# Optimization experiments

Measured on AMD Instinct MI355X. Metric: run time of the kernel, lower is better.

Reference implementation:

```python
import jax, jax.numpy as jnp
import numpy as np

N, E, B, DIM = 10000, 100000, 64, 64
NF, EF, H = 92, 50, 128
N_CONV, STEPS = 2, 2


def setup_inputs() -> dict:
    key = jax.random.key(0)
    ks = jax.random.split(key, 16)
    r = lambda k, s: jax.random.normal(k, s, dtype=jnp.float32) * 0.05
    return {
        "x": jax.random.normal(ks[0], (N, NF), dtype=jnp.float32),
        "edge_attr": jax.random.normal(ks[1], (E, EF), dtype=jnp.float32),
        "lin0_w": r(ks[2], (DIM, NF)), "lin0_b": jnp.zeros((DIM,), jnp.float32),
        "nn1_w": r(ks[3], (H, EF)), "nn1_b": jnp.zeros((H,), jnp.float32),
        "nn2_w": r(ks[4], (DIM * DIM, H)), "nn2_b": jnp.zeros((DIM * DIM,), jnp.float32),
        "root": r(ks[5], (DIM, DIM)), "conv_bias": jnp.zeros((DIM,), jnp.float32),
        "gru_w_ih": r(ks[6], (3 * DIM, DIM)), "gru_w_hh": r(ks[7], (3 * DIM, DIM)),
        "gru_b_ih": jnp.zeros((3 * DIM,), jnp.float32), "gru_b_hh": jnp.zeros((3 * DIM,), jnp.float32),
        "lstm_w_ih": r(ks[8], (4 * DIM, 2 * DIM)), "lstm_w_hh": r(ks[9], (4 * DIM, DIM)),
        "lstm_b_ih": jnp.zeros((4 * DIM,), jnp.float32), "lstm_b_hh": jnp.zeros((4 * DIM,), jnp.float32),
        "lin1_w": r(ks[10], (DIM, 2 * DIM)), "lin1_b": jnp.zeros((DIM,), jnp.float32),
        "lin2_w": r(ks[11], (1, DIM)), "lin2_b": jnp.zeros((1,), jnp.float32),
        "edge_index": jax.random.randint(ks[12], (2, E), 0, N),
        "batch": jnp.sort(jax.random.randint(ks[13], (N,), 0, B)),
    }


def _forward(x, edge_attr, lin0_w, lin0_b, nn1_w, nn1_b, nn2_w, nn2_b, root, conv_bias,
             gru_w_ih, gru_w_hh, gru_b_ih, gru_b_hh, lstm_w_ih, lstm_w_hh, lstm_b_ih, lstm_b_hh,
             lin1_w, lin1_b, lin2_w, lin2_b, edge_index, batch):
    src, dst = edge_index[0], edge_index[1]
    out = jax.nn.relu(x @ lin0_w.T + lin0_b)            # [N, DIM]
    h = out                                              # GRU hidden state (h0 = out)
    # Edge-conditioned weights depend only on edge_attr; identical each conv step.
    he = jax.nn.relu(edge_attr @ nn1_w.T + nn1_b)        # [E, H]
    We = (he @ nn2_w.T + nn2_b).reshape(E, DIM, DIM)     # [E, DIM, DIM]
    deg = jax.ops.segment_sum(jnp.ones((E,), jnp.float32), dst, num_segments=N)
    inv_deg = jnp.where(deg > 0, 1.0 / jnp.maximum(deg, 1.0), 0.0)[:, None]
    for _ in range(N_CONV):
        msg = jnp.einsum('ei,eio->eo', out[src], We)     # per-edge matvec, [E, DIM]
        agg = jax.ops.segment_sum(msg, dst, num_segments=N) * inv_deg  # scatter-mean
        m = jax.nn.relu(agg + out @ root + conv_bias)
        # GRU cell (torch gate order: r, z, n)
        gx = m @ gru_w_ih.T + gru_b_ih
        gh = h @ gru_w_hh.T + gru_b_hh
        xr, xz, xn = jnp.split(gx, 3, axis=-1)
        hr, hz, hn = jnp.split(gh, 3, axis=-1)
        rg = jax.nn.sigmoid(xr + hr)
        zg = jax.nn.sigmoid(xz + hz)
        ng = jnp.tanh(xn + rg * hn)
        h = (1.0 - zg) * ng + zg * h
        out = h
    # Set2Set pooling
    q_star = jnp.zeros((B, 2 * DIM), jnp.float32)
    hs = jnp.zeros((B, DIM), jnp.float32)
    cs = jnp.zeros((B, DIM), jnp.float32)
    for _ in range(STEPS):
        gates = q_star @ lstm_w_ih.T + lstm_b_ih + hs @ lstm_w_hh.T + lstm_b_hh
        ig, fg, gg, og = jnp.split(gates, 4, axis=-1)    # torch gate order i,f,g,o
        cs = jax.nn.sigmoid(fg) * cs + jax.nn.sigmoid(ig) * jnp.tanh(gg)
        hs = jax.nn.sigmoid(og) * jnp.tanh(cs)
        q = hs                                           # [B, DIM]
        e = jnp.sum(out * q[batch], axis=-1)             # [N]
        emax = jax.ops.segment_max(e, batch, num_segments=B)
        ee = jnp.exp(e - emax[batch])
        denom = jax.ops.segment_sum(ee, batch, num_segments=B)
        a = ee / jnp.maximum(denom, 1e-16)[batch]        # per-graph softmax
        rvec = jax.ops.segment_sum(a[:, None] * out, batch, num_segments=B)
        q_star = jnp.concatenate([q, rvec], axis=-1)     # [B, 2*DIM]
    y = jax.nn.relu(q_star @ lin1_w.T + lin1_b) @ lin2_w.T + lin2_b
    return y.reshape(-1)                                 # [B]


def reference(x, edge_attr, lin0_w, lin0_b, nn1_w, nn1_b, nn2_w, nn2_b, root, conv_bias,
              gru_w_ih, gru_w_hh, gru_b_ih, gru_b_hh, lstm_w_ih, lstm_w_hh, lstm_b_ih, lstm_b_hh,
              lin1_w, lin1_b, lin2_w, lin2_b, edge_index, batch):
    return _forward(x, edge_attr, lin0_w, lin0_b, nn1_w, nn1_b, nn2_w, nn2_b, root, conv_bias,
                    gru_w_ih, gru_w_hh, gru_b_ih, gru_b_hh, lstm_w_ih, lstm_w_hh, lstm_b_ih, lstm_b_hh,
                    lin1_w, lin1_b, lin2_w, lin2_b, edge_index, batch)
```

## Files before the change

kernel.cpp:

```cpp
#include <hip/hip_runtime.h>
#include <hip/hip_bf16.h>

#define N_   10000
#define E_   100000
#define B_   64
#define DIM_ 64
#define NF_  92
#define EF_  50
#define H_   128
#define NPAD 10048

typedef unsigned int u32;
typedef unsigned short u16;
typedef __attribute__((ext_vector_type(8))) short s16x8;
typedef __attribute__((ext_vector_type(4))) float f32x4;

__device__ __forceinline__ float sigm(float x) { return 1.f / (1.f + __expf(-x)); }
__device__ __forceinline__ float rdlane(float v, int l) {
  return __uint_as_float(__builtin_amdgcn_readlane(__float_as_uint(v), l));
}
__device__ __forceinline__ float bf2f(u16 u) {
  return __uint_as_float(((u32)u) << 16);
}
__device__ __forceinline__ u16 f2bf(float f) {
  u32 u = __float_as_uint(f);
  u32 r = (u + 0x7FFFu + ((u >> 16) & 1u)) >> 16;
  return (u16)r;
}

__global__ __launch_bounds__(256) void k_lin0(const float* __restrict__ x,
                                              const float* __restrict__ w,
                                              const float* __restrict__ b,
                                              float* __restrict__ out) {
  __shared__ float xs[4][NF_];
  __shared__ float w_s[DIM_][93];
  int n0 = blockIdx.x << 2;
  int tid = threadIdx.x;
  for (int k = tid; k < 4 * NF_; k += 256) {
    int nl = k / NF_, f = k % NF_;
    xs[nl][f] = x[(size_t)(n0 + nl) * NF_ + f];
  }
  for (int g = tid; g < DIM_ * NF_; g += 256) {
    int d = g / NF_, f = g % NF_;
    w_s[d][f] = w[g];
  }
  __syncthreads();
  int nl = tid >> 6, d = tid & 63;
  float acc = b[d];
  for (int f = 0; f < NF_; ++f) acc += xs[nl][f] * w_s[d][f];
  out[(size_t)(n0 + nl) * DIM_ + d] = fmaxf(acc, 0.f);
}

__global__ __launch_bounds__(256) void k_he(const float* __restrict__ ea,
                                            const float* __restrict__ w,
                                            const float* __restrict__ b,
                                            float* __restrict__ he) {
  __shared__ float wt[EF_][132];
  __shared__ float es[32][52];
  int e0 = blockIdx.x * 32, t = threadIdx.x;
  for (int g = t; g < H_ * EF_; g += 256) {
    int h = g / EF_, f = g % EF_;
    wt[f][h] = w[g];
  }
  for (int g = t; g < 32 * EF_; g += 256) {
    int e = g / EF_, f = g % EF_;
    es[e][f] = ea[(size_t)(e0 + e) * EF_ + f];
  }
  __syncthreads();
  int h0 = (t & 31) << 2, eg = t >> 5;
  float acc[4][4];
#pragma unroll
  for (int j = 0; j < 4; ++j)
#pragma unroll
    for (int c = 0; c < 4; ++c) acc[j][c] = b[h0 + c];
  for (int f = 0; f < EF_; ++f) {
    float4 wv = *(const float4*)&wt[f][h0];
    const float* wp = (const float*)&wv;
#pragma unroll
    for (int j = 0; j < 4; ++j) {
      float ev = es[eg * 4 + j][f];
#pragma unroll
      for (int c = 0; c < 4; ++c) acc[j][c] = fmaf(ev, wp[c], acc[j][c]);
    }
  }
#pragma unroll
  for (int j = 0; j < 4; ++j) {
    float4 o;
    o.x = fmaxf(acc[j][0], 0.f); o.y = fmaxf(acc[j][1], 0.f);
    o.z = fmaxf(acc[j][2], 0.f); o.w = fmaxf(acc[j][3], 0.f);
    *(float4*)&he[(size_t)(e0 + eg * 4 + j) * H_ + h0] = o;
  }
}

__global__ __launch_bounds__(256) void k_hist(const int* __restrict__ ei,
                                              int* __restrict__ outcnt,
                                              float* __restrict__ degf) {
  int e = blockIdx.x * 256 + threadIdx.x;
  if (e < E_) {
    atomicAdd(&outcnt[ei[e]], 1);
    atomicAdd(&degf[ei[E_ + e]], 1.0f);
  }
}

__global__ __launch_bounds__(1024) void k_scan(const int* __restrict__ outcnt,
                                               int* __restrict__ estart,
                                               int* __restrict__ cursor) {
  __shared__ int part[1024];
  int t = threadIdx.x;
  int base = t * 10;
  int c[10];
  int s = 0;
#pragma unroll
  for (int j = 0; j < 10; ++j) {
    int idx = base + j;
    c[j] = (idx < N_) ? outcnt[idx] : 0;
    s += c[j];
  }
  part[t] = s;
  __syncthreads();
  for (int off = 1; off < 1024; off <<= 1) {
    int v = (t >= off) ? part[t - off] : 0;
    __syncthreads();
    part[t] += v;
    __syncthreads();
  }
  int ex = (t > 0) ? part[t - 1] : 0;
#pragma unroll
  for (int j = 0; j < 10; ++j) {
    int idx = base + j;
    if (idx < N_) { estart[idx] = ex; cursor[idx] = ex; }
    ex += c[j];
  }
  if (t == 1023) estart[N_] = part[1023];
}

__global__ __launch_bounds__(256) void k_scatter(const int* __restrict__ ei,
                                                 int* __restrict__ cursor,
                                                 int* __restrict__ eorder) {
  int e = blockIdx.x * 256 + threadIdx.x;
  if (e < E_) {
    int s = ei[e];
    int pos = atomicAdd(&cursor[s], 1);
    eorder[pos] = e;
  }
}

__global__ __launch_bounds__(256) void k_gstart(const int* __restrict__ batch,
                                                int* __restrict__ gs) {
  int n = blockIdx.x * 256 + threadIdx.x;
  if (n >= N_) return;
  int b = batch[n];
  if (n == 0) {
    for (int bb = 0; bb <= b; ++bb) gs[bb] = 0;
  } else {
    int pb = batch[n - 1];
    if (pb != b)
      for (int bb = pb + 1; bb <= b; ++bb) gs[bb] = n;
  }
  if (n == N_ - 1) {
    for (int bb = b + 1; bb <= B_; ++bb) gs[bb] = N_;
  }
}

__global__ __launch_bounds__(256) void k_transpose(const float* __restrict__ gih,
                                                   const float* __restrict__ ghh,
                                                   const float* __restrict__ lih,
                                                   const float* __restrict__ lhh,
                                                   float* __restrict__ gihT,
                                                   float* __restrict__ ghhT,
                                                   float* __restrict__ lihT,
                                                   float* __restrict__ lhhT) {
  int idx = blockIdx.x * 256 + threadIdx.x;
  if (idx < 192 * 64) {
    int r = idx >> 6, i = idx & 63;
    gihT[i * 192 + r] = gih[idx];
    ghhT[i * 192 + r] = ghh[idx];
  }
  if (idx < 256 * 128) {
    int r = idx >> 7, k = idx & 127;
    lihT[k * 256 + r] = lih[idx];
  }
  if (idx < 256 * 64) {
    int r = idx >> 6, k = idx & 63;
    lhhT[k * 256 + r] = lhh[idx];
  }
}

__global__ __launch_bounds__(256) void k_prep_w(const float* __restrict__ w,
                                                u16* __restrict__ bth,
                                                u16* __restrict__ btl,
                                                int CW) {
  int idx = blockIdx.x * 256 + threadIdx.x;
  if (idx >= 64 * 64 * 128) return;
  int h = idx & 127;
  int io = idx >> 7;
  int o = io & 63;
  int i = io >> 6;
  int chunk = h / CW, hl = h % CW;
  float v = w[idx];
  u16 hh = f2bf(v);
  float r = v - bf2f(hh);
  size_t dst = (size_t)chunk * CW * 4096 + ((size_t)(hl * 64 + o)) * 64 + i;
  bth[dst] = hh;
  btl[dst] = f2bf(r);
}

__global__ __launch_bounds__(256) void k_split_a(const float* __restrict__ src,
                                                 u16* __restrict__ hi,
                                                 u16* __restrict__ lo) {
  int idx = blockIdx.x * 256 + threadIdx.x;
  if (idx >= NPAD * 64) return;
  float v = (idx < N_ * 64) ? src[idx] : 0.f;
  u16 h = f2bf(v);
  float r = v - bf2f(h);
  hi[idx] = h;
  lo[idx] = f2bf(r);
}

__global__ __launch_bounds__(256) void k_vgemm_mfma(const u16* __restrict__ Ah,
                                                    const u16* __restrict__ Al,
                                                    const u16* __restrict__ BTh,
                                                    const u16* __restrict__ BTl,
                                                    float* __restrict__ V4,
                                                    int H4Cb) {
  int n0 = blockIdx.x << 6;
  int by = blockIdx.y;
  int tid = threadIdx.x;
  int w = tid >> 6, l = tid & 63;
  int lr = l & 15, lg = l >> 4;
  int o0 = w << 4;
  int h0 = by << 2;
  f32x4 acc[4][4];
#pragma unroll
  for (int nt = 0; nt < 4; ++nt)
#pragma unroll
    for (int t = 0; t < 4; ++t) acc[nt][t] = (f32x4){0.f, 0.f, 0.f, 0.f};
#pragma unroll
  for (int ks = 0; ks < 2; ++ks) {
    int kk = (lg << 3) + (ks << 5);
    s16x8 ah[4], al[4];
#pragma unroll
    for (int nt = 0; nt < 4; ++nt) {
      size_t ao = (size_t)(n0 + (nt << 4) + lr) * 64 + kk;
      ah[nt] = *(const s16x8*)(Ah + ao);
      al[nt] = *(const s16x8*)(Al + ao);
    }
    s16x8 bh[4], bl[4];
#pragma unroll
    for (int t = 0; t < 4; ++t) {
      size_t bo = (size_t)(((h0 + t) << 6) + o0 + lr) * 64 + kk;
      bh[t] = *(const s16x8*)(BTh + bo);
      bl[t] = *(const s16x8*)(BTl + bo);
    }
#pragma unroll
    for (int nt = 0; nt < 4; ++nt)
#pragma unroll
      for (int t = 0; t < 4; ++t) {
        acc[nt][t] = __builtin_amdgcn_mfma_f32_16x16x32_bf16(ah[nt], bh[t], acc[nt][t], 0, 0, 0);
        acc[nt][t] = __builtin_amdgcn_mfma_f32_16x16x32_bf16(ah[nt], bl[t], acc[nt][t], 0, 0, 0);
        acc[nt][t] = __builtin_amdgcn_mfma_f32_16x16x32_bf16(al[nt], bh[t], acc[nt][t], 0, 0, 0);
      }
  }
  float4* out4 = (float4*)V4;
#pragma unroll
  for (int nt = 0; nt < 4; ++nt)
#pragma unroll
    for (int r = 0; r < 4; ++r) {
      int n = n0 + (nt << 4) + (lg << 2) + r;
      if (n < N_) {
        float4 f;
        f.x = acc[nt][0][r];
        f.y = acc[nt][1][r];
        f.z = acc[nt][2][r];
        f.w = acc[nt][3][r];
        out4[((size_t)n * H4Cb + by) * 64 + o0 + lr] = f;
      }
    }
}

__global__ __launch_bounds__(256) void k_bt(const float* __restrict__ out,
                                            const float* __restrict__ nn2b,
                                            float* __restrict__ bt) {
  __shared__ float os[4][64];
  int n0 = blockIdx.x << 2;
  int tid = threadIdx.x;
  int nl = tid >> 6, o = tid & 63;
  os[nl][o] = out[(size_t)(n0 + nl) * 64 + o];
  __syncthreads();
  float acc = 0.f;
  for (int i = 0; i < 64; ++i) acc += os[nl][i] * nn2b[(i << 6) + o];
  bt[(size_t)(n0 + nl) * 64 + o] = acc;
}

template <int H4C>
__global__ __launch_bounds__(256) void k_edge(const float* __restrict__ V4,
                                              const float* __restrict__ he,
                                              const float* __restrict__ bt,
                                              const int* __restrict__ ei,
                                              const int* __restrict__ estart,
                                              const int* __restrict__ eorder,
                                              float* __restrict__ agg,
                                              int hofs) {
  int wid = threadIdx.x >> 6, lane = threadIdx.x & 63;
  int n = blockIdx.x * 4 + wid;
  if (n >= N_) return;
  int se = estart[n], ee = estart[n + 1];
  if (se == ee) return;
  const float4* vp = (const float4*)V4 + (size_t)n * H4C * 64 + lane;
  float4 v4[H4C];
#pragma unroll
  for (int h4 = 0; h4 < H4C; ++h4) v4[h4] = vp[(size_t)h4 * 64];
  float btv = (hofs == 0) ? bt[(size_t)n * 64 + lane] : 0.f;
  constexpr int CWm1 = 4 * H4C - 1;
  for (int q = se; q < ee; ++q) {
    int eid = eorder[q];
    int dst = ei[E_ + eid];
    const float* hep = &he[(size_t)eid * H_];
    float hh, hh2 = 0.f;
    if (H4C == 32) { hh = hep[lane]; hh2 = hep[64 + lane]; }
    else           { hh = hep[hofs + (lane & CWm1)]; }
    float acc = btv;
#pragma unroll
    for (int h4 = 0; h4 < H4C; ++h4) {
      const float* vv = (const float*)&v4[h4];
#pragma unroll
      for (int c = 0; c < 4; ++c) {
        int hl = h4 * 4 + c;
        float bh = (hl < 64) ? rdlane(hh, hl) : rdlane(hh2, hl - 64);
        acc = fmaf(bh, vv[c], acc);
      }
    }
    atomicAdd(&agg[(size_t)dst * 64 + lane], acc);
  }
}

__global__ __launch_bounds__(256) void k_update(const float* __restrict__ agg,
                                                const float* __restrict__ deg,
                                                const float* __restrict__ cur,
                                                const float* __restrict__ root,
                                                const float* __restrict__ cbias,
                                                const float* __restrict__ wihT,
                                                const float* __restrict__ whhT,
                                                const float* __restrict__ bih,
                                                const float* __restrict__ bhh,
                                                float* __restrict__ nxt) {
  __shared__ float outs[32][64];
  __shared__ float ms[32][64];
  int n0 = blockIdx.x << 5;
  int tid = threadIdx.x;
  int o = tid & 63, g = tid >> 6;
#pragma unroll
  for (int k = 0; k < 8; ++k) {
    int idx = tid + (k << 8);
    int nl = idx >> 6, i = idx & 63;
    int n = n0 + nl;
    outs[nl][i] = (n < N_) ? cur[(size_t)n * 64 + i] : 0.f;
  }
  __syncthreads();
  float acc[8];
  float cb = cbias[o];
#pragma unroll
  for (int j = 0; j < 8; ++j) {
    int n = n0 + (g << 3) + j;
    if (n < N_) {
      float dg = deg[n];
      float iv = dg > 0.f ? 1.f / dg : 0.f;
      acc[j] = agg[(size_t)n * 64 + o] * iv + cb;
    } else acc[j] = 0.f;
  }
  for (int i = 0; i < 64; ++i) {
    float r = root[(i << 6) + o];
#pragma unroll
    for (int j = 0; j < 8; ++j) acc[j] = fmaf(outs[(g << 3) + j][i], r, acc[j]);
  }
#pragma unroll
  for (int j = 0; j < 8; ++j) ms[(g << 3) + j][o] = fmaxf(acc[j], 0.f);
  __syncthreads();
  float xr[8], xz[8], xn[8], hr[8], hz[8], hn[8];
  {
    float br = bih[o], bz = bih[64 + o], bn = bih[128 + o];
    float dr = bhh[o], dz = bhh[64 + o], dn = bhh[128 + o];
#pragma unroll
    for (int j = 0; j < 8; ++j) {
      xr[j] = br; xz[j] = bz; xn[j] = bn;
      hr[j] = dr; hz[j] = dz; hn[j] = dn;
    }
  }
  for (int i = 0; i < 64; ++i) {
    const float* wi = &wihT[i * 192];
    const float* vi = &whhT[i * 192];
    float w0 = wi[o], w1 = wi[64 + o], w2 = wi[128 + o];
    float v0 = vi[o], v1 = vi[64 + o], v2 = vi[128 + o];
#pragma unroll
    for (int j = 0; j < 8; ++j) {
      int nl = (g << 3) + j;
      float mi = ms[nl][i], hi = outs[nl][i];
      xr[j] = fmaf(mi, w0, xr[j]);
      xz[j] = fmaf(mi, w1, xz[j]);
      xn[j] = fmaf(mi, w2, xn[j]);
      hr[j] = fmaf(hi, v0, hr[j]);
      hz[j] = fmaf(hi, v1, hz[j]);
      hn[j] = fmaf(hi, v2, hn[j]);
    }
  }
#pragma unroll
  for (int j = 0; j < 8; ++j) {
    int nl = (g << 3) + j;
    int n = n0 + nl;
    if (n < N_) {
      float rg = sigm(xr[j] + hr[j]);
      float zg = sigm(xz[j] + hz[j]);
      float ng = tanhf(xn[j] + rg * hn[j]);
      nxt[(size_t)n * 64 + o] = (1.f - zg) * ng + zg * outs[nl][o];
    }
  }
}

__global__ __launch_bounds__(256) void k_s2s(const float* __restrict__ out,
                                             const int* __restrict__ gs,
                                             float* __restrict__ qstar,
                                             float* __restrict__ hs,
                                             float* __restrict__ cs,
                                             const float* __restrict__ lihT,
                                             const float* __restrict__ lhhT,
                                             const float* __restrict__ bih,
                                             const float* __restrict__ bhh,
                                             const float* __restrict__ w1,
                                             const float* __restrict__ b1,
                                             const float* __restrict__ w2,
                                             const float* __restrict__ b2,
                                             float* __restrict__ y, int dofinal) {
  int b = blockIdx.x, tid = threadIdx.x;
  __shared__ float qs[128];
  __shared__ float hss[64];
  __shared__ float gsh[256];
  __shared__ float qv[64];
  __shared__ float rv[64];
  __shared__ float wred[4];
  __shared__ float rred[4][64];
  if (tid < 128) qs[tid] = qstar[b * 128 + tid];
  else if (tid < 192) hss[tid - 128] = hs[b * 64 + (tid - 128)];
  __syncthreads();
  {
    int r = tid;
    float acc = bih[r] + bhh[r];
    for (int k = 0; k < 128; ++k) acc += qs[k] * lihT[k * 256 + r];
    for (int k = 0; k < 64; ++k) acc += hss[k] * lhhT[k * 256 + r];
    gsh[r] = acc;
  }
  __syncthreads();
  if (tid < 64) {
    float ig = sigm(gsh[tid]), fg = sigm(gsh[64 + tid]);
    float gg = tanhf(gsh[128 + tid]), og = sigm(gsh[192 + tid]);
    float c = fg * cs[b * 64 + tid] + ig * gg;
    cs[b * 64 + tid] = c;
    float hv = og * tanhf(c);
    hs[b * 64 + tid] = hv;
    qv[tid] = hv;
  }
  __syncthreads();
  int wid = tid >> 6, l = tid & 63;
  int s = gs[b], e_ = gs[b + 1];
  float wmax = -3.4e38f;
  for (int n = s + wid; n < e_; n += 4) {
    float p = out[(size_t)n * 64 + l] * qv[l];
#pragma unroll
    for (int off = 32; off; off >>= 1) p += __shfl_xor(p, off);
    wmax = fmaxf(wmax, p);
  }
  if (l == 0) wred[wid] = wmax;
  __syncthreads();
  float gmax = fmaxf(fmaxf(wred[0], wred[1]), fmaxf(wred[2], wred[3]));
  __syncthreads();
  float dacc = 0.f, racc = 0.f;
  for (int n = s + wid; n < e_; n += 4) {
    float p = out[(size_t)n * 64 + l] * qv[l];
#pragma unroll
    for (int off = 32; off; off >>= 1) p += __shfl_xor(p, off);
    float ee = __expf(p - gmax);
    dacc += ee;
    racc += ee * out[(size_t)n * 64 + l];
  }
  rred[wid][l] = racc;
  if (l == 0) wred[wid] = dacc;
  __syncthreads();
  if (wid == 0) {
    float denom = wred[0] + wred[1] + wred[2] + wred[3];
    float r = (rred[0][l] + rred[1][l] + rred[2][l] + rred[3][l]) /
              fmaxf(denom, 1e-16f);
    rv[l] = r;
    qstar[b * 128 + l] = qv[l];
    qstar[b * 128 + 64 + l] = r;
  }
  if (dofinal) {
    __syncthreads();
    if (tid < 64) {
      float acc = b1[tid];
      for (int k = 0; k < 64; ++k) acc += qv[k] * w1[tid * 128 + k];
      for (int k = 0; k < 64; ++k) acc += rv[k] * w1[tid * 128 + 64 + k];
      float t1 = fmaxf(acc, 0.f) * w2[tid];
#pragma unroll
      for (int off = 32; off; off >>= 1) t1 += __shfl_xor(t1, off);
      if (tid == 0) y[b] = t1 + b2[0];
    }
  }
}

extern "C" void kernel_launch(void* const* d_in, const int* in_sizes, int n_in,
                              void* d_out, int out_size, void* d_ws, size_t ws_size,
                              hipStream_t stream) {
  const float* x        = (const float*)d_in[0];
  const float* ea       = (const float*)d_in[1];
  const float* lin0_w   = (const float*)d_in[2];
  const float* lin0_b   = (const float*)d_in[3];
  const float* nn1_w    = (const float*)d_in[4];
  const float* nn1_b    = (const float*)d_in[5];
  const float* nn2_w    = (const float*)d_in[6];
  const float* nn2_b    = (const float*)d_in[7];
  const float* root     = (const float*)d_in[8];
  const float* cbias    = (const float*)d_in[9];
  const float* gru_wih  = (const float*)d_in[10];
  const float* gru_whh  = (const float*)d_in[11];
  const float* gru_bih  = (const float*)d_in[12];
  const float* gru_bhh  = (const float*)d_in[13];
  const float* lstm_wih = (const float*)d_in[14];
  const float* lstm_whh = (const float*)d_in[15];
  const float* lstm_bih = (const float*)d_in[16];
  const float* lstm_bhh = (const float*)d_in[17];
  const float* lin1_w   = (const float*)d_in[18];
  const float* lin1_b   = (const float*)d_in[19];
  const float* lin2_w   = (const float*)d_in[20];
  const float* lin2_b   = (const float*)d_in[21];
  const int*   ei       = (const int*)d_in[22];
  const int*   batch    = (const int*)d_in[23];
  float* yout = (float*)d_out;
  (void)n_in; (void)in_sizes; (void)out_size;

  size_t off = 0;
  auto carve = [&](size_t bytes) -> void* {
    void* p = (char*)d_ws + off;
    off = (off + bytes + 255) & ~(size_t)255;
    return p;
  };
  float* deg    = (float*)carve((size_t)N_ * 4);
  int*   outcnt = (int*)carve((size_t)N_ * 4);
  float* qstar  = (float*)carve((size_t)B_ * 128 * 4);
  float* hs     = (float*)carve((size_t)B_ * 64 * 4);
  float* cs     = (float*)carve((size_t)B_ * 64 * 4);
  size_t zero_span = off;
  float* out_a  = (float*)carve((size_t)N_ * DIM_ * 4);
  float* out_b  = (float*)carve((size_t)N_ * DIM_ * 4);
  float* bt     = (float*)carve((size_t)N_ * DIM_ * 4);
  float* agg    = (float*)carve((size_t)N_ * DIM_ * 4);
  int*   estart = (int*)carve((size_t)(N_ + 1) * 4);
  int*   cursor = (int*)carve((size_t)N_ * 4);
  int*   eorder = (int*)carve((size_t)E_ * 4);
  int*   gs     = (int*)carve((size_t)(B_ + 1) * 4);
  float* gihT   = (float*)carve((size_t)192 * 64 * 4);
  float* ghhT   = (float*)carve((size_t)192 * 64 * 4);
  float* lihT   = (float*)carve((size_t)256 * 128 * 4);
  float* lhhT   = (float*)carve((size_t)256 * 64 * 4);
  u16*   Ah     = (u16*)carve((size_t)NPAD * 64 * 2);
  u16*   Al     = (u16*)carve((size_t)NPAD * 64 * 2);
  u16*   BTh    = (u16*)carve((size_t)128 * 4096 * 2);
  u16*   BTl    = (u16*)carve((size_t)128 * 4096 * 2);
  float* he     = (float*)carve((size_t)E_ * H_ * 4);
  size_t common = off;
  int CW = 8;
  {
    const int cws[4] = {64, 32, 16, 8};
    for (int i = 0; i < 4; ++i) {
      size_t vb = (size_t)N_ * cws[i] * 64 * 4;
      if (common + vb <= ws_size) { CW = cws[i]; break; }
    }
  }
  float* V4 = (float*)carve((size_t)N_ * CW * 64 * 4);
  int nchunks = 128 / CW;
  int H4Cb = CW / 4;

  hipMemsetAsync(d_ws, 0, zero_span, stream);

  k_lin0<<<N_ / 4, 256, 0, stream>>>(x, lin0_w, lin0_b, out_a);
  k_he<<<E_ / 32, 256, 0, stream>>>(ea, nn1_w, nn1_b, he);
  k_hist<<<(E_ + 255) / 256, 256, 0, stream>>>(ei, outcnt, deg);
  k_scan<<<1, 1024, 0, stream>>>(outcnt, estart, cursor);
  k_scatter<<<(E_ + 255) / 256, 256, 0, stream>>>(ei, cursor, eorder);
  k_gstart<<<(N_ + 255) / 256, 256, 0, stream>>>(batch, gs);
  k_transpose<<<128, 256, 0, stream>>>(gru_wih, gru_whh, lstm_wih, lstm_whh,
                                       gihT, ghhT, lihT, lhhT);
  k_prep_w<<<2048, 256, 0, stream>>>(nn2_w, BTh, BTl, CW);

  float* cur = out_a;
  float* nxt = out_b;
  int egrid = (N_ + 3) / 4;
  int nblk = NPAD / 64;
  for (int t = 0; t < 2; ++t) {
    hipMemsetAsync(agg, 0, (size_t)N_ * DIM_ * 4, stream);
    k_bt<<<N_ / 4, 256, 0, stream>>>(cur, nn2_b, bt);
    k_split_a<<<(NPAD * 64 + 255) / 256, 256, 0, stream>>>(cur, Ah, Al);
    for (int chunk = 0; chunk < nchunks; ++chunk) {
      int h_base = chunk * CW;
      size_t boff = (size_t)chunk * CW * 4096;
      dim3 vg(nblk, H4Cb);
      k_vgemm_mfma<<<vg, 256, 0, stream>>>(Ah, Al, BTh + boff, BTl + boff, V4, H4Cb);
      switch (CW) {
        case 64:  k_edge<16><<<egrid, 256, 0, stream>>>(V4, he, bt, ei, estart, eorder, agg, h_base); break;
        case 32:  k_edge<8><<<egrid, 256, 0, stream>>>(V4, he, bt, ei, estart, eorder, agg, h_base); break;
        case 16:  k_edge<4><<<egrid, 256, 0, stream>>>(V4, he, bt, ei, estart, eorder, agg, h_base); break;
        default:  k_edge<2><<<egrid, 256, 0, stream>>>(V4, he, bt, ei, estart, eorder, agg, h_base); break;
      }
    }
    k_update<<<(N_ + 31) / 32, 256, 0, stream>>>(agg, deg, cur, root, cbias,
                                                 gihT, ghhT, gru_bih, gru_bhh, nxt);
    float* tmp = cur; cur = nxt; nxt = tmp;
  }

  k_s2s<<<B_, 256, 0, stream>>>(cur, gs, qstar, hs, cs, lihT, lhhT,
                                lstm_bih, lstm_bhh, lin1_w, lin1_b, lin2_w,
                                lin2_b, yout, 0);
  k_s2s<<<B_, 256, 0, stream>>>(cur, gs, qstar, hs, cs, lihT, lhhT,
                                lstm_bih, lstm_bhh, lin1_w, lin1_b, lin2_w,
                                lin2_b, yout, 1);
}
```

Before: 817.8 us.

## Store edge hidden features chunk-major in source-sorted order and prefetch in edge loop

The edge MLP output is now written directly into a chunk-major layout ordered by each edge's position in the source-sorted edge list, and destination indices are pre-sorted the same way. The edge kernel then reads contiguous hidden-feature and destination streams instead of indirecting through an edge-order array into a strided per-edge row. The next edge's features and destination are software-prefetched while the current edge is processed. This removes a gather level and improves coalescing, at the cost of running k_he after the scatter and adding an extra position array.

```diff
diff --git a/kernel.cpp b/kernel.cpp
--- a/kernel.cpp
+++ b/kernel.cpp
@@ -51,47 +51,6 @@
   out[(size_t)(n0 + nl) * DIM_ + d] = fmaxf(acc, 0.f);
 }
 
-__global__ __launch_bounds__(256) void k_he(const float* __restrict__ ea,
-                                            const float* __restrict__ w,
-                                            const float* __restrict__ b,
-                                            float* __restrict__ he) {
-  __shared__ float wt[EF_][132];
-  __shared__ float es[32][52];
-  int e0 = blockIdx.x * 32, t = threadIdx.x;
-  for (int g = t; g < H_ * EF_; g += 256) {
-    int h = g / EF_, f = g % EF_;
-    wt[f][h] = w[g];
-  }
-  for (int g = t; g < 32 * EF_; g += 256) {
-    int e = g / EF_, f = g % EF_;
-    es[e][f] = ea[(size_t)(e0 + e) * EF_ + f];
-  }
-  __syncthreads();
-  int h0 = (t & 31) << 2, eg = t >> 5;
-  float acc[4][4];
-#pragma unroll
-  for (int j = 0; j < 4; ++j)
-#pragma unroll
-    for (int c = 0; c < 4; ++c) acc[j][c] = b[h0 + c];
-  for (int f = 0; f < EF_; ++f) {
-    float4 wv = *(const float4*)&wt[f][h0];
-    const float* wp = (const float*)&wv;
-#pragma unroll
-    for (int j = 0; j < 4; ++j) {
-      float ev = es[eg * 4 + j][f];
-#pragma unroll
-      for (int c = 0; c < 4; ++c) acc[j][c] = fmaf(ev, wp[c], acc[j][c]);
-    }
-  }
-#pragma unroll
-  for (int j = 0; j < 4; ++j) {
-    float4 o;
-    o.x = fmaxf(acc[j][0], 0.f); o.y = fmaxf(acc[j][1], 0.f);
-    o.z = fmaxf(acc[j][2], 0.f); o.w = fmaxf(acc[j][3], 0.f);
-    *(float4*)&he[(size_t)(e0 + eg * 4 + j) * H_ + h0] = o;
-  }
-}
-
 __global__ __launch_bounds__(256) void k_hist(const int* __restrict__ ei,
                                               int* __restrict__ outcnt,
                                               float* __restrict__ degf) {
@@ -136,12 +95,62 @@
 
 __global__ __launch_bounds__(256) void k_scatter(const int* __restrict__ ei,
                                                  int* __restrict__ cursor,
-                                                 int* __restrict__ eorder) {
+                                                 int* __restrict__ epos,
+                                                 int* __restrict__ dst_s) {
   int e = blockIdx.x * 256 + threadIdx.x;
   if (e < E_) {
     int s = ei[e];
     int pos = atomicAdd(&cursor[s], 1);
-    eorder[pos] = e;
+    epos[e] = pos;
+    dst_s[pos] = ei[E_ + e];
+  }
+}
+
+__global__ __launch_bounds__(256) void k_he(const float* __restrict__ ea,
+                                            const float* __restrict__ w,
+                                            const float* __restrict__ b,
+                                            float* __restrict__ he_s,
+                                            const int* __restrict__ epos,
+                                            int lcw) {
+  __shared__ float wt[EF_][132];
+  __shared__ float es[32][52];
+  int e0 = blockIdx.x * 32, t = threadIdx.x;
+  for (int g = t; g < H_ * EF_; g += 256) {
+    int h = g / EF_, f = g % EF_;
+    wt[f][h] = w[g];
+  }
+  for (int g = t; g < 32 * EF_; g += 256) {
+    int e = g / EF_, f = g % EF_;
+    es[e][f] = ea[(size_t)(e0 + e) * EF_ + f];
+  }
+  __syncthreads();
+  int h0 = (t & 31) << 2, eg = t >> 5;
+  float acc[4][4];
+#pragma unroll
+  for (int j = 0; j < 4; ++j)
+#pragma unroll
+    for (int c = 0; c < 4; ++c) acc[j][c] = b[h0 + c];
+  for (int f = 0; f < EF_; ++f) {
+    float4 wv = *(const float4*)&wt[f][h0];
+    const float* wp = (const float*)&wv;
+#pragma unroll
+    for (int j = 0; j < 4; ++j) {
+      float ev = es[eg * 4 + j][f];
+#pragma unroll
+      for (int c = 0; c < 4; ++c) acc[j][c] = fmaf(ev, wp[c], acc[j][c]);
+    }
+  }
+  int cwm1 = (1 << lcw) - 1;
+#pragma unroll
+  for (int j = 0; j < 4; ++j) {
+    float4 o;
+    o.x = fmaxf(acc[j][0], 0.f); o.y = fmaxf(acc[j][1], 0.f);
+    o.z = fmaxf(acc[j][2], 0.f); o.w = fmaxf(acc[j][3], 0.f);
+    int e = e0 + eg * 4 + j;
+    int pos = epos[e];
+    int chunk = h0 >> lcw;
+    int hl = h0 & cwm1;
+    *(float4*)&he_s[(((size_t)chunk * E_ + pos) << lcw) + hl] = o;
   }
 }
 
@@ -294,13 +303,13 @@
 
 template <int H4C>
 __global__ __launch_bounds__(256) void k_edge(const float* __restrict__ V4,
-                                              const float* __restrict__ he,
+                                              const float* __restrict__ heq,
                                               const float* __restrict__ bt,
-                                              const int* __restrict__ ei,
+                                              const int* __restrict__ dst_s,
                                               const int* __restrict__ estart,
-                                              const int* __restrict__ eorder,
                                               float* __restrict__ agg,
-                                              int hofs) {
+                                              int addbt) {
+  constexpr int CW = 4 * H4C;
   int wid = threadIdx.x >> 6, lane = threadIdx.x & 63;
   int n = blockIdx.x * 4 + wid;
   if (n >= N_) return;
@@ -310,27 +319,31 @@
   float4 v4[H4C];
 #pragma unroll
   for (int h4 = 0; h4 < H4C; ++h4) v4[h4] = vp[(size_t)h4 * 64];
-  float btv = (hofs == 0) ? bt[(size_t)n * 64 + lane] : 0.f;
-  constexpr int CWm1 = 4 * H4C - 1;
+#pragma unroll
+  for (int h4 = 0; h4 < H4C; ++h4)
+    asm volatile("" : "+v"(v4[h4].x), "+v"(v4[h4].y), "+v"(v4[h4].z), "+v"(v4[h4].w));
+  float btv = addbt ? bt[(size_t)n * 64 + lane] : 0.f;
+  int hl = lane & (CW - 1);
+  float hh = heq[(size_t)se * CW + hl];
+  int dst = dst_s[se];
   for (int q = se; q < ee; ++q) {
-    int eid = eorder[q];
-    int dst = ei[E_ + eid];
-    const float* hep = &he[(size_t)eid * H_];
-    float hh, hh2 = 0.f;
-    if (H4C == 32) { hh = hep[lane]; hh2 = hep[64 + lane]; }
-    else           { hh = hep[hofs + (lane & CWm1)]; }
+    float hc = hh;
+    int dc = dst;
+    if (q + 1 < ee) {
+      hh = heq[(size_t)(q + 1) * CW + hl];
+      dst = dst_s[q + 1];
+    }
     float acc = btv;
 #pragma unroll
     for (int h4 = 0; h4 < H4C; ++h4) {
-      const float* vv = (const float*)&v4[h4];
+      const float* vv = &v4[h4].x;
 #pragma unroll
       for (int c = 0; c < 4; ++c) {
-        int hl = h4 * 4 + c;
-        float bh = (hl < 64) ? rdlane(hh, hl) : rdlane(hh2, hl - 64);
+        float bh = rdlane(hc, h4 * 4 + c);
         acc = fmaf(bh, vv[c], acc);
       }
     }
-    atomicAdd(&agg[(size_t)dst * 64 + lane], acc);
+    atomicAdd(&agg[(size_t)dc * 64 + lane], acc);
   }
 }
 
@@ -554,7 +567,8 @@
   float* agg    = (float*)carve((size_t)N_ * DIM_ * 4);
   int*   estart = (int*)carve((size_t)(N_ + 1) * 4);
   int*   cursor = (int*)carve((size_t)N_ * 4);
-  int*   eorder = (int*)carve((size_t)E_ * 4);
+  int*   epos   = (int*)carve((size_t)E_ * 4);
+  int*   dst_s  = (int*)carve((size_t)E_ * 4);
   int*   gs     = (int*)carve((size_t)(B_ + 1) * 4);
   float* gihT   = (float*)carve((size_t)192 * 64 * 4);
   float* ghhT   = (float*)carve((size_t)192 * 64 * 4);
@@ -564,7 +578,7 @@
   u16*   Al     = (u16*)carve((size_t)NPAD * 64 * 2);
   u16*   BTh    = (u16*)carve((size_t)128 * 4096 * 2);
   u16*   BTl    = (u16*)carve((size_t)128 * 4096 * 2);
-  float* he     = (float*)carve((size_t)E_ * H_ * 4);
+  float* he_s   = (float*)carve((size_t)E_ * H_ * 4);
   size_t common = off;
   int CW = 8;
   {
@@ -576,15 +590,16 @@
   }
   float* V4 = (float*)carve((size_t)N_ * CW * 64 * 4);
   int nchunks = 128 / CW;
+  int lcw = __builtin_ctz(CW);
   int H4Cb = CW / 4;
 
   hipMemsetAsync(d_ws, 0, zero_span, stream);
 
   k_lin0<<<N_ / 4, 256, 0, stream>>>(x, lin0_w, lin0_b, out_a);
-  k_he<<<E_ / 32, 256, 0, stream>>>(ea, nn1_w, nn1_b, he);
   k_hist<<<(E_ + 255) / 256, 256, 0, stream>>>(ei, outcnt, deg);
   k_scan<<<1, 1024, 0, stream>>>(outcnt, estart, cursor);
-  k_scatter<<<(E_ + 255) / 256, 256, 0, stream>>>(ei, cursor, eorder);
+  k_scatter<<<(E_ + 255) / 256, 256, 0, stream>>>(ei, cursor, epos, dst_s);
+  k_he<<<E_ / 32, 256, 0, stream>>>(ea, nn1_w, nn1_b, he_s, epos, lcw);
   k_gstart<<<(N_ + 255) / 256, 256, 0, stream>>>(batch, gs);
   k_transpose<<<128, 256, 0, stream>>>(gru_wih, gru_whh, lstm_wih, lstm_whh,
                                        gihT, ghhT, lihT, lhhT);
@@ -599,15 +614,16 @@
     k_bt<<<N_ / 4, 256, 0, stream>>>(cur, nn2_b, bt);
     k_split_a<<<(NPAD * 64 + 255) / 256, 256, 0, stream>>>(cur, Ah, Al);
     for (int chunk = 0; chunk < nchunks; ++chunk) {
-      int h_base = chunk * CW;
       size_t boff = (size_t)chunk * CW * 4096;
+      const float* heq = he_s + (size_t)chunk * E_ * CW;
       dim3 vg(nblk, H4Cb);
       k_vgemm_mfma<<<vg, 256, 0, stream>>>(Ah, Al, BTh + boff, BTl + boff, V4, H4Cb);
+      int addbt = (chunk == 0) ? 1 : 0;
       switch (CW) {
-        case 64:  k_edge<16><<<egrid, 256, 0, stream>>>(V4, he, bt, ei, estart, eorder, agg, h_base); break;
-        case 32:  k_edge<8><<<egrid, 256, 0, stream>>>(V4, he, bt, ei, estart, eorder, agg, h_base); break;
-        case 16:  k_edge<4><<<egrid, 256, 0, stream>>>(V4, he, bt, ei, estart, eorder, agg, h_base); break;
-        default:  k_edge<2><<<egrid, 256, 0, stream>>>(V4, he, bt, ei, estart, eorder, agg, h_base); break;
+        case 64:  k_edge<16><<<egrid, 256, 0, stream>>>(V4, heq, bt, dst_s, estart, agg, addbt); break;
+        case 32:  k_edge<8><<<egrid, 256, 0, stream>>>(V4, heq, bt, dst_s, estart, agg, addbt); break;
+        case 16:  k_edge<4><<<egrid, 256, 0, stream>>>(V4, heq, bt, dst_s, estart, agg, addbt); break;
+        default:  k_edge<2><<<egrid, 256, 0, stream>>>(V4, heq, bt, dst_s, estart, agg, addbt); break;
       }
     }
     k_update<<<(N_ + 31) / 32, 256, 0, stream>>>(agg, deg, cur, root, cbias,
```

Measured after the change: 792.1 us. 1.03x faster.
